# Kernel tuning notes

Measured on AMD Instinct MI355X. Metric: run time of the kernel, lower is better.

The kernel has to match this reference:

```python
import jax, jax.numpy as jnp
import numpy as np


def setup_inputs() -> dict:
    key = jax.random.key(0)
    k1, k2 = jax.random.split(key)
    x = jax.random.normal(k1, (16, 4096, 256), dtype=jnp.float32)
    embedding = jax.random.normal(k2, (1024, 256), dtype=jnp.float32)
    return {"x": x, "embedding": embedding}


def reference(x, embedding):
    # which_dim = -1 (default): no permute.
    shape = x.shape
    xf = x.reshape(-1, shape[-1])  # [N, D]
    x_sq = jnp.sum(xf * xf, axis=-1, keepdims=True)          # [N, 1]
    e_sq = jnp.sum(embedding * embedding, axis=-1)           # [K]
    dist = -(x_sq - 2.0 * (xf @ embedding.T) + e_sq[None, :])  # [N, K]
    embed_indices = jnp.argmax(dist, axis=1)                 # [N]
    embed_indices = embed_indices.reshape(shape[:-1])        # [B, S]
    quantization = embedding[embed_indices]                  # [B, S, D]
    return (quantization, embed_indices)
```

## Files before the change

### kernel.cpp

```cpp
#include <hip/hip_runtime.h>
#include <hip/hip_fp16.h>
#include <math.h>

#define MROWS   65536
#define NCODES  1024
#define KD      256
#define MARGIN  0.25f

typedef unsigned short u16;
typedef __attribute__((ext_vector_type(8))) _Float16 hfrag;
typedef __attribute__((ext_vector_type(4))) float f32x4;

#define IOFF ((size_t)MROWS * KD)

__device__ __forceinline__ float addrn(float a, float b) {
    float d; asm("v_add_f32 %0, %1, %2" : "=v"(d) : "v"(a), "v"(b)); return d;
}

__device__ __forceinline__ float sumsq_vf8ic4(const float* __restrict__ xr) {
    float a[4][8];
#pragma unroll
    for (int i = 0; i < 4; ++i)
#pragma unroll
        for (int l = 0; l < 8; ++l) a[i][l] = 0.f;
#pragma unroll
    for (int m = 0; m < 8; ++m)
#pragma unroll
        for (int i = 0; i < 4; ++i)
#pragma unroll
            for (int l = 0; l < 8; ++l) {
                float v = xr[m * 32 + i * 8 + l];
                a[i][l] = fmaf(v, v, a[i][l]);
            }
    float cc[8];
#pragma unroll
    for (int l = 0; l < 8; ++l)
        cc[l] = addrn(addrn(addrn(a[0][l], a[1][l]), a[2][l]), a[3][l]);
    float u0 = addrn(cc[0], cc[4]), u1 = addrn(cc[1], cc[5]);
    float u2 = addrn(cc[2], cc[6]), u3 = addrn(cc[3], cc[7]);
    return addrn(addrn(u0, u2), addrn(u1, u3));
}

__global__ __launch_bounds__(256)
void vq_pack(const float* __restrict__ src, u16* __restrict__ dh) {
    __shared__ __align__(16) float lx[16 * 260];
    const int t = threadIdx.x;
    const size_t base = (size_t)blockIdx.x * 16 * 256;
#pragma unroll
    for (int qq = 0; qq < 4; ++qq) {
        int i4 = qq * 256 + t;
        int row = i4 >> 6, col = (i4 & 63) * 4;
        *(float4*)(lx + row * 260 + col) = *(const float4*)(src + base + (size_t)i4 * 4);
    }
    __syncthreads();
#pragma unroll
    for (int i = 0; i < 2; ++i) {
        int s = t + 256 * i;
        int kb = s >> 6, lane = s & 63;
        int r = lane & 15, kg = lane >> 4;
        int k0 = kb * 32 + kg * 8;
        u16 vh[8];
#pragma unroll
        for (int j = 0; j < 8; ++j) {
            float v = lx[r * 260 + k0 + j];
            vh[j] = __half_as_ushort(__float2half(v));
        }
        size_t off = (((size_t)blockIdx.x * 8 + kb) * 64 + lane) * 8;
        *(ulonglong2*)(dh + off) = *(ulonglong2*)vh;
    }
}

__global__ __launch_bounds__(256)
void vq_prep_emb(const float* __restrict__ emb, u16* __restrict__ Eh,
                 float* __restrict__ esq, float* __restrict__ embT,
                 unsigned int* __restrict__ cnt) {
    if (blockIdx.x == 0 && threadIdx.x == 0) *cnt = 0;
    __shared__ float lx[64 * 257];
    const int t = threadIdx.x;
    const int c0 = blockIdx.x * 64;
    const size_t base = (size_t)c0 * 256;
#pragma unroll
    for (int qq = 0; qq < 16; ++qq) {
        int idx4 = qq * 256 + t;
        int row = idx4 >> 6, col4 = idx4 & 63;
        *(float4*)(lx + row * 257 + col4 * 4) = *(const float4*)(emb + base + (size_t)idx4 * 4);
    }
    __syncthreads();
    if (t < 64) esq[c0 + t] = sumsq_vf8ic4(lx + t * 257);
#pragma unroll
    for (int i = 0; i < 8; ++i) {
        int s = i * 256 + t;
        int fl = s >> 6, lane = s & 63;
        int rb_l = fl >> 3, kb = fl & 7;
        int r = rb_l * 16 + (lane & 15), kg = lane >> 4;
        int k0 = kb * 32 + kg * 8;
        u16 vh[8];
#pragma unroll
        for (int j = 0; j < 8; ++j)
            vh[j] = __half_as_ushort(__float2half(lx[r * 257 + k0 + j]));
        size_t off = (((size_t)(blockIdx.x * 4 + rb_l) * 8 + kb) * 64 + lane) * 8;
        *(ulonglong2*)(Eh + off) = *(ulonglong2*)vh;
    }
#pragma unroll
    for (int i = 0; i < 64; ++i) {
        int k = i * 4 + (t >> 6), col = t & 63;
        embT[(size_t)k * 1024 + c0 + col] = lx[col * 257 + k];
    }
}

__global__ __launch_bounds__(256, 2)
void vq_gemm(const u16* __restrict__ Ah, const u16* __restrict__ Eh,
             const float* __restrict__ esq, float* __restrict__ tw) {
    extern __shared__ u16 ldsA[];
    const int t = threadIdx.x;
    const int wave = t >> 6, lane = t & 63;
    const int wm = wave >> 1, wn = wave & 1;
    const int q = lane >> 4, c = lane & 15;
    const int m0 = blockIdx.x * 128;
    const int mrb8 = blockIdx.x * 64;

#pragma unroll
    for (int u = 0; u < 16; ++u) {
        int f = wave * 16 + u;
        const u16* srcp = Ah + ((size_t)(mrb8 + f) * 64 + lane) * 8;
        __builtin_amdgcn_global_load_lds((const unsigned int*)srcp,
                                         (unsigned int*)(ldsA + f * 512), 16, 0, 0);
    }
    __syncthreads();

    auto LOADB = [&](int s, hfrag* dst) {
        const int f0 = ((s >> 3) * 64) + (wn * 4) * 8 + (s & 7);
#pragma unroll
        for (int ni = 0; ni < 4; ++ni)
            dst[ni] = *(const hfrag*)(Eh + (size_t)(f0 + ni * 8) * 512 + lane * 8);
    };
    auto LDA = [&](int s, hfrag* dst) {
        const int ks = s & 7;
#pragma unroll
        for (int mi = 0; mi < 4; ++mi)
            dst[mi] = *(const hfrag*)(ldsA + ((wm * 4 + mi) * 8 + ks) * 512 + lane * 8);
    };

    float b1[16], s2v[16], bi[16];
#pragma unroll
    for (int r = 0; r < 16; ++r) { b1[r] = INFINITY; s2v[r] = INFINITY; bi[r] = 0.f; }

    f32x4 acc[4][4];
#pragma unroll
    for (int mi = 0; mi < 4; ++mi)
#pragma unroll
        for (int ni = 0; ni < 4; ++ni) acc[mi][ni] = 0.f;

    hfrag bA[4], bB[4];
    LOADB(0, bA);
    LOADB(1, bB);

    for (int sp = 0; sp < 32; ++sp) {
        const int s0 = sp * 2, s1 = sp * 2 + 1;
        {
            hfrag nx[4];
            LOADB(s0 + 2 < 64 ? s0 + 2 : 0, nx);
            hfrag af[4];
            LDA(s0, af);
#pragma unroll
            for (int mi = 0; mi < 4; ++mi)
#pragma unroll
                for (int ni = 0; ni < 4; ++ni)
                    acc[mi][ni] = __builtin_amdgcn_mfma_f32_16x16x32_f16(af[mi], bA[ni], acc[mi][ni], 0, 0, 0);
#pragma unroll
            for (int ni = 0; ni < 4; ++ni) bA[ni] = nx[ni];
        }
        {
            hfrag nx[4];
            LOADB(s1 + 2 < 64 ? s1 + 2 : 0, nx);
            hfrag af[4];
            LDA(s1, af);
#pragma unroll
            for (int mi = 0; mi < 4; ++mi)
#pragma unroll
                for (int ni = 0; ni < 4; ++ni)
                    acc[mi][ni] = __builtin_amdgcn_mfma_f32_16x16x32_f16(af[mi], bB[ni], acc[mi][ni], 0, 0, 0);
#pragma unroll
            for (int ni = 0; ni < 4; ++ni) bB[ni] = nx[ni];
        }
        if ((s1 & 7) == 7) {
            const int nqi = s1 >> 3;
#pragma unroll
            for (int ni = 0; ni < 4; ++ni) {
                const int code = nqi * 128 + wn * 64 + ni * 16 + c;
                const float e2 = esq[code];
                const float ci = (float)code;
#pragma unroll
                for (int mi = 0; mi < 4; ++mi)
#pragma unroll
                    for (int j = 0; j < 4; ++j) {
                        const int r = mi * 4 + j;
                        float sc = fmaf(-2.f, acc[mi][ni][j], e2);
                        bool lt = sc < b1[r];
                        s2v[r] = fminf(s2v[r], lt ? b1[r] : sc);
                        if (lt) { b1[r] = sc; bi[r] = ci; }
                    }
            }
#pragma unroll
            for (int mi = 0; mi < 4; ++mi)
#pragma unroll
                for (int ni = 0; ni < 4; ++ni) acc[mi][ni] = 0.f;
        }
    }

#pragma unroll
    for (int r = 0; r < 16; ++r) {
#pragma unroll
        for (int mm = 1; mm < 16; mm <<= 1) {
            float ob = __shfl_xor(b1[r], mm, 64);
            float os = __shfl_xor(s2v[r], mm, 64);
            float oi = __shfl_xor(bi[r], mm, 64);
            if (ob < b1[r]) { s2v[r] = fminf(b1[r], os); b1[r] = ob; bi[r] = oi; }
            else            { s2v[r] = fminf(s2v[r], ob); }
        }
    }
    __syncthreads();
    float* sm = (float*)ldsA;
    if (c == 0) {
#pragma unroll
        for (int mi = 0; mi < 4; ++mi)
#pragma unroll
            for (int j = 0; j < 4; ++j) {
                int r = mi * 4 + j;
                int row_l = wm * 64 + mi * 16 + q * 4 + j;
                sm[row_l * 6 + wn * 3 + 0] = b1[r];
                sm[row_l * 6 + wn * 3 + 1] = s2v[r];
                sm[row_l * 6 + wn * 3 + 2] = bi[r];
            }
    }
    __syncthreads();
    if (t < 128) {
        float b0 = sm[t * 6 + 0], sA = sm[t * 6 + 1], i0 = sm[t * 6 + 2];
        float bb = sm[t * 6 + 3], sB = sm[t * 6 + 4], i1 = sm[t * 6 + 5];
        float b, s2, bidx;
        if (b0 <= bb) { b = b0; bidx = i0; s2 = fminf(sA, bb); }
        else          { b = bb; bidx = i1; s2 = fminf(sB, b0); }
        size_t row = (size_t)(m0 + t);
        tw[row * 4 + 0] = b;
        tw[row * 4 + 1] = s2;
        tw[row * 4 + 2] = bidx;
    }
}

__global__ __launch_bounds__(256)
void vq_flag_gather(const float* __restrict__ tw, const float* __restrict__ emb,
                    float* __restrict__ idxf, float* __restrict__ quant,
                    unsigned int* __restrict__ cnt, int* __restrict__ list) {
    __shared__ int idx_l[64];
    const int t = threadIdx.x;
    const int r0 = blockIdx.x * 64;
    if (t < 64) {
        int row = r0 + t;
        float b  = tw[(size_t)row * 4 + 0];
        float s2 = tw[(size_t)row * 4 + 1];
        int bidx = (int)tw[(size_t)row * 4 + 2];
        idxf[row] = (float)bidx;
        idx_l[t] = bidx;
        if (s2 - b < MARGIN) {
            unsigned int pos = atomicAdd(cnt, 1u);
            list[pos] = row;
        }
    }
    __syncthreads();
    const int lane = t & 63, w = t >> 6;
#pragma unroll
    for (int u = 0; u < 16; ++u) {
        int rl = u * 4 + w;
        int idx = idx_l[rl];
        *(float4*)(quant + (size_t)(r0 + rl) * 256 + lane * 4) =
            *(const float4*)(emb + (size_t)idx * 256 + lane * 4);
    }
}

__global__ __launch_bounds__(256)
void vq_refine1(const float* __restrict__ x, const float* __restrict__ emb,
                const float* __restrict__ embT, const float* __restrict__ esq,
                const int* __restrict__ list, const unsigned int* __restrict__ cnt,
                float* __restrict__ idxf, float* __restrict__ quant) {
    __shared__ __align__(16) float xs[8][260];
    __shared__ float xsq_s[8];
    __shared__ float lb[8][4];
    __shared__ int   li[8][4];
    __shared__ int   li2[8];
    const int t = threadIdx.x;
    const int wave = t >> 6, lane = t & 63;
    const unsigned int n = *cnt;
    float e2q[4];
#pragma unroll
    for (int qq = 0; qq < 4; ++qq) e2q[qq] = esq[qq * 256 + t];

    for (unsigned int g = blockIdx.x; g * 8u < n; g += gridDim.x) {
        const unsigned int r0 = g * 8u;
        const int nr = (int)min(8u, n - r0);
        __syncthreads();
#pragma unroll
        for (int u = 0; u < 2; ++u) {
            int s = u * 256 + t;
            int rr = s >> 6, l4 = s & 63;
            if (rr < nr) {
                int row = list[r0 + rr];
                *(float4*)(&xs[rr][l4 * 4]) = *(const float4*)(x + (size_t)row * 256 + l4 * 4);
            }
        }
        __syncthreads();
        if (t < nr) xsq_s[t] = sumsq_vf8ic4(&xs[t][0]);
        __syncthreads();

        float d[8][4];
#pragma unroll
        for (int r = 0; r < 8; ++r)
#pragma unroll
            for (int qq = 0; qq < 4; ++qq) d[r][qq] = 0.f;

        for (int kq = 0; kq < 64; ++kq) {
            float ev[4][4];
#pragma unroll
            for (int j = 0; j < 4; ++j)
#pragma unroll
                for (int qq = 0; qq < 4; ++qq)
                    ev[qq][j] = embT[(size_t)(kq * 4 + j) * 1024 + qq * 256 + t];
            float4 xf[8];
#pragma unroll
            for (int r = 0; r < 8; ++r) xf[r] = *(const float4*)(&xs[r][kq * 4]);
#pragma unroll
            for (int r = 0; r < 8; ++r)
#pragma unroll
                for (int qq = 0; qq < 4; ++qq) {
                    d[r][qq] = fmaf(xf[r].x, ev[qq][0], d[r][qq]);
                    d[r][qq] = fmaf(xf[r].y, ev[qq][1], d[r][qq]);
                    d[r][qq] = fmaf(xf[r].z, ev[qq][2], d[r][qq]);
                    d[r][qq] = fmaf(xf[r].w, ev[qq][3], d[r][qq]);
                }
        }
#pragma unroll
        for (int r = 0; r < 8; ++r) {
            float sv = INFINITY; int bc = 0x7fffffff;
#pragma unroll
            for (int qq = 0; qq < 4; ++qq) {
                float s = addrn(fmaf(-2.f, d[r][qq], xsq_s[r]), e2q[qq]);
                if (s < sv) { sv = s; bc = qq * 256 + t; }
            }
#pragma unroll
            for (int mm = 1; mm < 64; mm <<= 1) {
                float ob = __shfl_xor(sv, mm, 64);
                int oi = __shfl_xor(bc, mm, 64);
                if (ob < sv || (ob == sv && oi < bc)) { sv = ob; bc = oi; }
            }
            if (lane == 0) { lb[r][wave] = sv; li[r][wave] = bc; }
        }
        __syncthreads();
        if (t < nr) {
            float best = lb[t][0]; int bix = li[t][0];
#pragma unroll
            for (int w = 1; w < 4; ++w) {
                float ob = lb[t][w]; int oi = li[t][w];
                if (ob < best || (ob == best && oi < bix)) { best = ob; bix = oi; }
            }
            idxf[list[r0 + t]] = (float)bix;
            li2[t] = bix;
        }
        __syncthreads();
#pragma unroll
        for (int rr = 0; rr < 2; ++rr) {
            int rl = wave * 2 + rr;
            if (rl < nr) {
                int row = list[r0 + rl];
                int idx = li2[rl];
                *(float4*)(quant + (size_t)row * 256 + lane * 4) =
                    *(const float4*)(emb + (size_t)idx * 256 + lane * 4);
            }
        }
    }
}

extern "C" void kernel_launch(void* const* d_in, const int* in_sizes, int n_in,
                              void* d_out, int out_size, void* d_ws, size_t ws_size,
                              hipStream_t stream) {
    const float* x   = (const float*)d_in[0];
    const float* emb = (const float*)d_in[1];
    float* out  = (float*)d_out;
    float* idxf = out + IOFF;

    u16* Ah = (u16*)out;

    char* ws = (char*)d_ws;
    u16* Eh    = (u16*)(ws);
    float* esq = (float*)(ws + (512 << 10));
    unsigned int* cnt = (unsigned int*)(ws + (640 << 10));
    int* list  = (int*)(ws + (640 << 10) + 256);
    float* embT = (float*)(ws + (1 << 20));
    float* tw   = (float*)(ws + (2 << 20));

    vq_prep_emb<<<dim3(16), dim3(256), 0, stream>>>(emb, Eh, esq, embT, cnt);
    vq_pack<<<dim3(MROWS / 16), dim3(256), 0, stream>>>(x, Ah);
    vq_gemm<<<dim3(MROWS / 128), dim3(256), 65536, stream>>>(Ah, Eh, esq, tw);
    vq_flag_gather<<<dim3(MROWS / 64), dim3(256), 0, stream>>>(tw, emb, idxf, out, cnt, list);
    vq_refine1<<<dim3(512), dim3(256), 0, stream>>>(x, emb, embT, esq, list, cnt, idxf, out);
}
```

Before: 133.7 us.

## Double-buffer accumulators to overlap argmin epilogue with MFMA, fuse flagging into GEMM

```diff
diff --git a/kernel.cpp b/kernel.cpp
--- a/kernel.cpp
+++ b/kernel.cpp
@@ -110,7 +110,8 @@
 
 __global__ __launch_bounds__(256, 2)
 void vq_gemm(const u16* __restrict__ Ah, const u16* __restrict__ Eh,
-             const float* __restrict__ esq, float* __restrict__ tw) {
+             const float* __restrict__ esq, float* __restrict__ idxf,
+             unsigned int* __restrict__ cnt, int* __restrict__ list) {
     extern __shared__ u16 ldsA[];
     const int t = threadIdx.x;
     const int wave = t >> 6, lane = t & 63;
@@ -128,14 +129,13 @@
     }
     __syncthreads();
 
-    auto LOADB = [&](int s, hfrag* dst) {
-        const int f0 = ((s >> 3) * 64) + (wn * 4) * 8 + (s & 7);
+    auto LOADB = [&](int s, hfrag (&dst)[4]) {
+        const int f0 = ((s >> 3) * 64) + wn * 32 + (s & 7);
 #pragma unroll
         for (int ni = 0; ni < 4; ++ni)
             dst[ni] = *(const hfrag*)(Eh + (size_t)(f0 + ni * 8) * 512 + lane * 8);
     };
-    auto LDA = [&](int s, hfrag* dst) {
-        const int ks = s & 7;
+    auto LDA = [&](int ks, hfrag (&dst)[4]) {
 #pragma unroll
         for (int mi = 0; mi < 4; ++mi)
             dst[mi] = *(const hfrag*)(ldsA + ((wm * 4 + mi) * 8 + ks) * 512 + lane * 8);
@@ -145,68 +145,72 @@
 #pragma unroll
     for (int r = 0; r < 16; ++r) { b1[r] = INFINITY; s2v[r] = INFINITY; bi[r] = 0.f; }
 
-    f32x4 acc[4][4];
-#pragma unroll
-    for (int mi = 0; mi < 4; ++mi)
-#pragma unroll
-        for (int ni = 0; ni < 4; ++ni) acc[mi][ni] = 0.f;
-
     hfrag bA[4], bB[4];
     LOADB(0, bA);
     LOADB(1, bB);
 
-    for (int sp = 0; sp < 32; ++sp) {
-        const int s0 = sp * 2, s1 = sp * 2 + 1;
-        {
-            hfrag nx[4];
-            LOADB(s0 + 2 < 64 ? s0 + 2 : 0, nx);
-            hfrag af[4];
-            LDA(s0, af);
+    const f32x4 Z = {0.f, 0.f, 0.f, 0.f};
+
+    auto PASS = [&](int p, f32x4 (&acc)[4][4]) {
+#pragma unroll
+        for (int k2 = 0; k2 < 4; ++k2) {
+            const int ks0 = k2 * 2, ks1 = ks0 + 1;
+            const int s0 = p * 8 + ks0, s1 = s0 + 1;
+            {
+                hfrag nx[4]; LOADB(s0 + 2, nx);
+                hfrag af[4]; LDA(ks0, af);
+#pragma unroll
+                for (int mi = 0; mi < 4; ++mi)
+#pragma unroll
+                    for (int ni = 0; ni < 4; ++ni)
+                        acc[mi][ni] = __builtin_amdgcn_mfma_f32_16x16x32_f16(
+                            af[mi], bA[ni], (k2 == 0) ? Z : acc[mi][ni], 0, 0, 0);
+#pragma unroll
+                for (int ni = 0; ni < 4; ++ni) bA[ni] = nx[ni];
+            }
+            {
+                hfrag nx[4]; LOADB(s1 + 2, nx);
+                hfrag af[4]; LDA(ks1, af);
+#pragma unroll
+                for (int mi = 0; mi < 4; ++mi)
+#pragma unroll
+                    for (int ni = 0; ni < 4; ++ni)
+                        acc[mi][ni] = __builtin_amdgcn_mfma_f32_16x16x32_f16(af[mi], bB[ni], acc[mi][ni], 0, 0, 0);
+#pragma unroll
+                for (int ni = 0; ni < 4; ++ni) bB[ni] = nx[ni];
+            }
+        }
+    };
+    auto EPI = [&](int p, f32x4 (&acc)[4][4]) {
+#pragma unroll
+        for (int ni = 0; ni < 4; ++ni) {
+            const int code = p * 128 + wn * 64 + ni * 16 + c;
+            const float e2 = esq[code];
+            const float ci = (float)code;
 #pragma unroll
             for (int mi = 0; mi < 4; ++mi)
 #pragma unroll
-                for (int ni = 0; ni < 4; ++ni)
-                    acc[mi][ni] = __builtin_amdgcn_mfma_f32_16x16x32_f16(af[mi], bA[ni], acc[mi][ni], 0, 0, 0);
-#pragma unroll
-            for (int ni = 0; ni < 4; ++ni) bA[ni] = nx[ni];
-        }
-        {
-            hfrag nx[4];
-            LOADB(s1 + 2 < 64 ? s1 + 2 : 0, nx);
-            hfrag af[4];
-            LDA(s1, af);
-#pragma unroll
-            for (int mi = 0; mi < 4; ++mi)
-#pragma unroll
-                for (int ni = 0; ni < 4; ++ni)
-                    acc[mi][ni] = __builtin_amdgcn_mfma_f32_16x16x32_f16(af[mi], bB[ni], acc[mi][ni], 0, 0, 0);
-#pragma unroll
-            for (int ni = 0; ni < 4; ++ni) bB[ni] = nx[ni];
-        }
-        if ((s1 & 7) == 7) {
-            const int nqi = s1 >> 3;
-#pragma unroll
-            for (int ni = 0; ni < 4; ++ni) {
-                const int code = nqi * 128 + wn * 64 + ni * 16 + c;
-                const float e2 = esq[code];
-                const float ci = (float)code;
-#pragma unroll
-                for (int mi = 0; mi < 4; ++mi)
-#pragma unroll
-                    for (int j = 0; j < 4; ++j) {
-                        const int r = mi * 4 + j;
-                        float sc = fmaf(-2.f, acc[mi][ni][j], e2);
-                        bool lt = sc < b1[r];
-                        s2v[r] = fminf(s2v[r], lt ? b1[r] : sc);
-                        if (lt) { b1[r] = sc; bi[r] = ci; }
-                    }
-            }
-#pragma unroll
-            for (int mi = 0; mi < 4; ++mi)
-#pragma unroll
-                for (int ni = 0; ni < 4; ++ni) acc[mi][ni] = 0.f;
-        }
-    }
+                for (int j = 0; j < 4; ++j) {
+                    const int r = mi * 4 + j;
+                    float sc = fmaf(-2.f, acc[mi][ni][j], e2);
+                    bool lt = sc < b1[r];
+                    s2v[r] = fminf(s2v[r], lt ? b1[r] : sc);
+                    if (lt) { b1[r] = sc; bi[r] = ci; }
+                }
+        }
+    };
+
+    f32x4 accA[4][4], accB[4][4];
+    PASS(0, accA);
+    for (int h = 0; h < 3; ++h) {
+        PASS(2 * h + 1, accB);
+        EPI(2 * h, accA);
+        PASS(2 * h + 2, accA);
+        EPI(2 * h + 1, accB);
+    }
+    PASS(7, accB);
+    EPI(6, accA);
+    EPI(7, accB);
 
 #pragma unroll
     for (int r = 0; r < 16; ++r) {
@@ -240,38 +244,25 @@
         float b, s2, bidx;
         if (b0 <= bb) { b = b0; bidx = i0; s2 = fminf(sA, bb); }
         else          { b = bb; bidx = i1; s2 = fminf(sB, b0); }
-        size_t row = (size_t)(m0 + t);
-        tw[row * 4 + 0] = b;
-        tw[row * 4 + 1] = s2;
-        tw[row * 4 + 2] = bidx;
-    }
-}
-
-__global__ __launch_bounds__(256)
-void vq_flag_gather(const float* __restrict__ tw, const float* __restrict__ emb,
-                    float* __restrict__ idxf, float* __restrict__ quant,
-                    unsigned int* __restrict__ cnt, int* __restrict__ list) {
-    __shared__ int idx_l[64];
-    const int t = threadIdx.x;
-    const int r0 = blockIdx.x * 64;
-    if (t < 64) {
-        int row = r0 + t;
-        float b  = tw[(size_t)row * 4 + 0];
-        float s2 = tw[(size_t)row * 4 + 1];
-        int bidx = (int)tw[(size_t)row * 4 + 2];
-        idxf[row] = (float)bidx;
-        idx_l[t] = bidx;
+        int row = m0 + t;
+        idxf[row] = bidx;
         if (s2 - b < MARGIN) {
             unsigned int pos = atomicAdd(cnt, 1u);
             list[pos] = row;
         }
     }
-    __syncthreads();
+}
+
+__global__ __launch_bounds__(256)
+void vq_gather(const float* __restrict__ idxf, const float* __restrict__ emb,
+               float* __restrict__ quant) {
+    const int t = threadIdx.x;
+    const int r0 = blockIdx.x * 64;
     const int lane = t & 63, w = t >> 6;
 #pragma unroll
     for (int u = 0; u < 16; ++u) {
         int rl = u * 4 + w;
-        int idx = idx_l[rl];
+        int idx = (int)idxf[r0 + rl];
         *(float4*)(quant + (size_t)(r0 + rl) * 256 + lane * 4) =
             *(const float4*)(emb + (size_t)idx * 256 + lane * 4);
     }
@@ -394,11 +385,10 @@
     unsigned int* cnt = (unsigned int*)(ws + (640 << 10));
     int* list  = (int*)(ws + (640 << 10) + 256);
     float* embT = (float*)(ws + (1 << 20));
-    float* tw   = (float*)(ws + (2 << 20));
 
     vq_prep_emb<<<dim3(16), dim3(256), 0, stream>>>(emb, Eh, esq, embT, cnt);
     vq_pack<<<dim3(MROWS / 16), dim3(256), 0, stream>>>(x, Ah);
-    vq_gemm<<<dim3(MROWS / 128), dim3(256), 65536, stream>>>(Ah, Eh, esq, tw);
-    vq_flag_gather<<<dim3(MROWS / 64), dim3(256), 0, stream>>>(tw, emb, idxf, out, cnt, list);
+    vq_gemm<<<dim3(MROWS / 128), dim3(256), 65536, stream>>>(Ah, Eh, esq, idxf, cnt, list);
+    vq_gather<<<dim3(MROWS / 64), dim3(256), 0, stream>>>(idxf, emb, out);
     vq_refine1<<<dim3(512), dim3(256), 0, stream>>>(x, emb, embT, esq, list, cnt, idxf, out);
 }
```

Result: slower. 241.7 us (+80.7%).
